# Performance work log

Hardware: AMD Instinct MI355X
Metric: run time of the kernel (lower is better)

## Reference

```python
import jax, jax.numpy as jnp
import numpy as np

B, L, C, R = 8192, 49, 512, 128  # L = 7*7 hardcoded in module
H = W = 7


def _conv2d(x, w, b, pad):
    # x: (B, Cin, H, W), w: (Cout, Cin, k, k)
    y = jax.lax.conv_general_dilated(
        x, w, window_strides=(1, 1), padding=[(pad, pad), (pad, pad)],
        dimension_numbers=("NCHW", "OIHW", "NCHW"))
    return y + b[None, :, None, None]


def _star_relu(x, scale, bias):
    r = jnp.maximum(x, 0.0)
    return scale * (r * r) + bias


def setup_inputs() -> dict:
    key = jax.random.key(0)
    ks = jax.random.split(key, 12)
    s = 0.05
    return {
        "x": jax.random.normal(ks[0], (B, L, C), jnp.float32),
        "g_reduce_w": jax.random.normal(ks[1], (R, C), jnp.float32) * s,
        "l_reduce_w": jax.random.normal(ks[2], (R, C), jnp.float32) * s,
        "conv3_w": jax.random.normal(ks[3], (R // 2, R // 2, 3, 3), jnp.float32) * s,
        "conv3_b": jax.random.normal(ks[4], (R // 2,), jnp.float32) * s,
        "conv5_w": jax.random.normal(ks[5], (R - R // 2, R - R // 2, 5, 5), jnp.float32) * s,
        "conv5_b": jax.random.normal(ks[6], (R - R // 2,), jnp.float32) * s,
        "channel_w": jax.random.normal(ks[7], (C, R), jnp.float32) * s,
        "channel_b": jax.random.normal(ks[8], (C,), jnp.float32) * s,
        "spatial_w": jax.random.normal(ks[9], (1, 3 * R), jnp.float32) * s,
        "spatial_b": jax.random.normal(ks[10], (1,), jnp.float32) * s,
        "star_scale": jnp.ones((1,), jnp.float32),
        "star_bias": jnp.zeros((1,), jnp.float32),
    }


def reference(x, g_reduce_w, l_reduce_w, conv3_w, conv3_b, conv5_w, conv5_b,
              channel_w, channel_b, spatial_w, spatial_b, star_scale, star_bias):
    # x: (B, L, C) with L = 49 (7x7)
    # Global dual pooling over spatial (== over L)
    x_max = jnp.max(x, axis=1)   # (B, C)
    x_avg = jnp.mean(x, axis=1)  # (B, C)
    # g_reduce 1x1 conv (no bias) + StarReLU
    g1 = _star_relu(x_max @ g_reduce_w.T, star_scale, star_bias)  # (B, R)
    g2 = _star_relu(x_avg @ g_reduce_w.T, star_scale, star_bias)  # (B, R)
    # Local branch: 1x1 reduce -> HybConv2d (split 3x3 / 5x5) -> StarReLU
    x_img = x.transpose(0, 2, 1).reshape(B, C, H, W)
    x_l = jnp.einsum("bchw,rc->brhw", x_img, l_reduce_w)  # (B, R, 7, 7)
    xl1, xl2 = x_l[:, :R // 2], x_l[:, R // 2:]
    y1 = _conv2d(xl1, conv3_w, conv3_b, pad=1)
    y2 = _conv2d(xl2, conv5_w, conv5_b, pad=2)
    x_l = _star_relu(jnp.concatenate([y1, y2], axis=1), star_scale, star_bias)
    x_l = x_l.reshape(B, R, L).transpose(0, 2, 1)  # (B, L, R)
    # Channel gate: Linear(R->C) applied to each pooled branch, summed
    c_aggr = jax.nn.sigmoid((g1 @ channel_w.T + channel_b)
                            + (g2 @ channel_w.T + channel_b))  # (B, C)
    # Spatial gate: concat [x_l, g1 broadcast, g2 broadcast] -> Linear(3R->1)
    g1b = jnp.broadcast_to(g1[:, None, :], (B, L, R))
    g2b = jnp.broadcast_to(g2[:, None, :], (B, L, R))
    s_cat = jnp.concatenate([x_l, g1b, g2b], axis=-1)  # (B, L, 3R)
    s_aggr = jax.nn.sigmoid(jnp.einsum("blk,ok->blo", s_cat, spatial_w) + spatial_b)  # (B, L, 1)
    aggr = c_aggr[:, None, :] * s_aggr  # (B, L, C)
    return x * aggr
```

## Files before the change

### kernel.cpp

```cpp
#include <hip/hip_runtime.h>
#include <math.h>

#define B_ 8192
#define L_ 49
#define C_ 512
#define R_ 128

typedef short   bf16x8 __attribute__((ext_vector_type(8)));
typedef unsigned short u16x8 __attribute__((ext_vector_type(8)));
typedef float   f32x4  __attribute__((ext_vector_type(4)));

#define WS_LWF   0
#define WS_WB3F  65536
#define WS_WB5F  102400
#define WS_GWF   204800
#define WS_CWF   270336

#define SM_XB    0
#define SM_XLB   25088
#define SM_MAXB  25088
#define SM_SUMF  29184
#define SM_GA    37888
#define SM_G     38912
#define SM_CA    39936
#define SM_SPW   41984
#define SM_SP    44032
#define SM_GDOT  44288
#define SM_TOT   44304

__device__ __forceinline__ float bf2f(unsigned short u) {
    union { float f; unsigned int i; } v; v.i = ((unsigned int)u) << 16; return v.f;
}
__device__ __forceinline__ unsigned short f2bf(float f) {
    union { float f; unsigned int i; } v; v.f = f;
    unsigned int r = v.i + 0x7fffu + ((v.i >> 16) & 1u);
    return (unsigned short)(r >> 16);
}
__device__ __forceinline__ float star_relu(float x, float sc, float bi) {
    float r = fmaxf(x, 0.f);
    return sc * r * r + bi;
}
__device__ __forceinline__ float sigmoidf_(float x) {
    return 1.f / (1.f + __expf(-x));
}

__global__ void cvt_weights(const float* __restrict__ lw, const float* __restrict__ w3,
                            const float* __restrict__ w5, const float* __restrict__ gw,
                            const float* __restrict__ cw, unsigned short* __restrict__ ws)
{
    int t = blockIdx.x * blockDim.x + threadIdx.x;
    int stride = gridDim.x * blockDim.x;
    for (int i = t; i < 65536; i += stride) {
        int j = i & 7, lane = (i >> 3) & 63, ks = (i >> 9) & 15, nt = i >> 13;
        int n = nt * 16 + (lane & 15);
        int k = ks * 32 + (lane >> 4) * 8 + j;
        ws[WS_LWF + i] = f2bf(lw[n * 512 + k]);
        ws[WS_GWF + i] = f2bf(gw[n * 512 + k]);
    }
    for (int i = t; i < 65536; i += stride) {
        int j = i & 7, c = (i >> 3) & 511, r8 = i >> 12;
        ws[WS_CWF + i] = f2bf(cw[c * 128 + r8 * 8 + j]);
    }
    for (int i = t; i < 36864; i += stride) {
        int j = i & 7, lane = (i >> 3) & 63, ks = (i >> 9) & 1, f = (i >> 10) & 3, tap = i >> 12;
        int oc = f * 16 + (lane & 15);
        int ic = ks * 32 + (lane >> 4) * 8 + j;
        ws[WS_WB3F + i] = f2bf(w3[(oc * 64 + ic) * 9 + tap]);
    }
    for (int i = t; i < 102400; i += stride) {
        int j = i & 7, lane = (i >> 3) & 63, ks = (i >> 9) & 1, f = (i >> 10) & 3, tap = i >> 12;
        int oc = f * 16 + (lane & 15);
        int ic = ks * 32 + (lane >> 4) * 8 + j;
        ws[WS_WB5F + i] = f2bf(w5[(oc * 64 + ic) * 25 + tap]);
    }
}

template <int NTAP, int KD, int PAD, int COLBASE>
__device__ __forceinline__ void conv_mfma(const unsigned short* __restrict__ s_xlb,
                                          const unsigned short* __restrict__ wtbf,
                                          int m16, int kg, int ln, int f, f32x4 C[4])
{
    int lp_[4], i_[4], j_[4];
    #pragma unroll
    for (int mf = 0; mf < 4; ++mf) {
        lp_[mf] = mf * 16 + m16;
        i_[mf] = lp_[mf] / 7;
        j_[mf] = lp_[mf] % 7;
    }
    bf16x8 cur0 = *(const bf16x8*)(wtbf + ((0 * 4 + f) * 2 + 0) * 512 + ln * 8);
    bf16x8 cur1 = *(const bf16x8*)(wtbf + ((0 * 4 + f) * 2 + 1) * 512 + ln * 8);
    #pragma unroll
    for (int tap = 0; tap < NTAP; ++tap) {
        bf16x8 nxt0 = cur0, nxt1 = cur1;
        if (tap + 1 < NTAP) {
            nxt0 = *(const bf16x8*)(wtbf + (((tap + 1) * 4 + f) * 2 + 0) * 512 + ln * 8);
            nxt1 = *(const bf16x8*)(wtbf + (((tap + 1) * 4 + f) * 2 + 1) * 512 + ln * 8);
        }
        const int dy = tap / KD - PAD, dx = tap % KD - PAD;
        int lc[4];
        #pragma unroll
        for (int mf = 0; mf < 4; ++mf) {
            int ii = i_[mf] + dy, jj = j_[mf] + dx;
            bool v = (lp_[mf] < 49) & (ii >= 0) & (ii < 7) & (jj >= 0) & (jj < 7);
            lc[mf] = v ? (ii * 7 + jj) : 49;
        }
        #pragma unroll
        for (int mf = 0; mf < 4; ++mf) {
            int chunk0 = ((COLBASE >> 3) + kg) ^ (lc[mf] & 7);
            bf16x8 a = *(const bf16x8*)&s_xlb[lc[mf] * 128 + chunk0 * 8];
            C[mf] = __builtin_amdgcn_mfma_f32_16x16x32_bf16(a, cur0, C[mf], 0, 0, 0);
        }
        #pragma unroll
        for (int mf = 0; mf < 4; ++mf) {
            int chunk1 = ((COLBASE >> 3) + 4 + kg) ^ (lc[mf] & 7);
            bf16x8 a = *(const bf16x8*)&s_xlb[lc[mf] * 128 + chunk1 * 8];
            C[mf] = __builtin_amdgcn_mfma_f32_16x16x32_bf16(a, cur1, C[mf], 0, 0, 0);
        }
        cur0 = nxt0; cur1 = nxt1;
    }
}

__global__ __launch_bounds__(512, 4)
void mafn_fused(const float* __restrict__ x,
                const float* __restrict__ b3, const float* __restrict__ b5,
                const float* __restrict__ cb, const float* __restrict__ sw,
                const float* __restrict__ sb, const float* __restrict__ ssc,
                const float* __restrict__ sbi,
                const unsigned short* __restrict__ ws,
                float* __restrict__ out)
{
    __shared__ __align__(16) unsigned char smem[SM_TOT];
    unsigned short* s_xb   = (unsigned short*)(smem + SM_XB);
    unsigned short* s_xlb  = (unsigned short*)(smem + SM_XLB);
    unsigned short* s_maxb = (unsigned short*)(smem + SM_MAXB);
    float*          s_sumf = (float*)(smem + SM_SUMF);
    unsigned short* s_ga   = (unsigned short*)(smem + SM_GA);
    float*          s_g    = (float*)(smem + SM_G);
    float*          s_ca   = (float*)(smem + SM_CA);
    float*          s_spw  = (float*)(smem + SM_SPW);
    float*          s_sp   = (float*)(smem + SM_SP);
    float*          s_gdot = (float*)(smem + SM_GDOT);

    const int b = blockIdx.x, t = threadIdx.x;
    const int wv = t >> 6, ln = t & 63;
    const int m16 = ln & 15, kg = ln >> 4;
    const float scale = ssc[0], sbias = sbi[0];

    const unsigned short* lwf  = ws + WS_LWF;
    const unsigned short* wb3f = ws + WS_WB3F;
    const unsigned short* wb5f = ws + WS_WB5F;
    const unsigned short* gwf  = ws + WS_GWF;
    const unsigned short* cwf  = ws + WS_CWF;

    f32x4 accA[4];
    f32x4 accG;
    {
        const f32x4 z = {0.f, 0.f, 0.f, 0.f};
        #pragma unroll
        for (int mf = 0; mf < 4; ++mf) accA[mf] = z;
        accG = z;
    }

    const int l0 = wv * 6;
    const int nl = (wv < 7) ? 6 : 7;

    #pragma unroll 1
    for (int h = 0; h < 2; ++h) {
        {
            const float4* x4 = (const float4*)(x + (size_t)b * (L_ * C_)) + h * 64;
            float4 mx = {-3.4e38f, -3.4e38f, -3.4e38f, -3.4e38f};
            float4 sm = {0.f, 0.f, 0.f, 0.f};
            for (int li = 0; li < nl; ++li) {
                int l = l0 + li;
                float4 v = x4[l * 128 + ln];
                mx.x = fmaxf(mx.x, v.x); mx.y = fmaxf(mx.y, v.y);
                mx.z = fmaxf(mx.z, v.z); mx.w = fmaxf(mx.w, v.w);
                sm.x += v.x; sm.y += v.y; sm.z += v.z; sm.w += v.w;
                ushort4 p;
                p.x = f2bf(v.x); p.y = f2bf(v.y); p.z = f2bf(v.z); p.w = f2bf(v.w);
                int chunk = (ln >> 1) ^ (l & 7);
                *(ushort4*)&s_xb[l * 256 + chunk * 8 + (ln & 1) * 4] = p;
            }
            ushort4 pm;
            pm.x = f2bf(mx.x); pm.y = f2bf(mx.y); pm.z = f2bf(mx.z); pm.w = f2bf(mx.w);
            *(ushort4*)&s_maxb[wv * 256 + ln * 4] = pm;
            *(float4*)&s_sumf[wv * 256 + ln * 4] = sm;
        }
        __syncthreads();

        {
            if (t < 256) {
                int c = t;
                float m = bf2f(s_maxb[c]);
                #pragma unroll
                for (int i = 1; i < 8; ++i) m = fmaxf(m, bf2f(s_maxb[i * 256 + c]));
                s_ga[c] = f2bf(m);
            } else {
                int c = t - 256;
                float s = 0.f;
                #pragma unroll
                for (int i = 0; i < 8; ++i) s += s_sumf[i * 256 + c];
                s_ga[256 + c] = f2bf(s * (1.f / 49.f));
            }
        }
        __syncthreads();

        {
            int rowA[4];
            #pragma unroll
            for (int mf = 0; mf < 4; ++mf) rowA[mf] = min(mf * 16 + m16, 48);

            bf16x8 bb0 = *(const bf16x8*)(lwf + (wv * 16 + h * 8 + 0) * 512 + ln * 8);
            bf16x8 bb1 = *(const bf16x8*)(lwf + (wv * 16 + h * 8 + 1) * 512 + ln * 8);
            #pragma unroll
            for (int ks = 0; ks < 8; ++ks) {
                bf16x8 bn = bb1;
                if (ks + 2 < 8)
                    bn = *(const bf16x8*)(lwf + (wv * 16 + h * 8 + ks + 2) * 512 + ln * 8);
                #pragma unroll
                for (int mf = 0; mf < 4; ++mf) {
                    int chunk = (ks * 4 + kg) ^ (rowA[mf] & 7);
                    bf16x8 a = *(const bf16x8*)&s_xb[rowA[mf] * 256 + chunk * 8];
                    accA[mf] = __builtin_amdgcn_mfma_f32_16x16x32_bf16(a, bb0, accA[mf], 0, 0, 0);
                }
                bb0 = bb1; bb1 = bn;
            }

            bf16x8 gb0 = *(const bf16x8*)(gwf + (wv * 16 + h * 8 + 0) * 512 + ln * 8);
            bf16x8 gb1 = *(const bf16x8*)(gwf + (wv * 16 + h * 8 + 1) * 512 + ln * 8);
            const bf16x8 zz = {0,0,0,0,0,0,0,0};
            #pragma unroll
            for (int ks = 0; ks < 8; ++ks) {
                bf16x8 gn = gb1;
                if (ks + 2 < 8)
                    gn = *(const bf16x8*)(gwf + (wv * 16 + h * 8 + ks + 2) * 512 + ln * 8);
                bf16x8 a = (m16 < 2) ? *(const bf16x8*)&s_ga[m16 * 256 + ks * 32 + kg * 8] : zz;
                accG = __builtin_amdgcn_mfma_f32_16x16x32_bf16(a, gb0, accG, 0, 0, 0);
                gb0 = gb1; gb1 = gn;
            }
        }
        __syncthreads();
    }

    {
        if (t < 64) ((unsigned int*)(s_xlb + 49 * 128))[t] = 0;
        const int n = wv * 16 + m16;
        #pragma unroll
        for (int mf = 0; mf < 4; ++mf) {
            #pragma unroll
            for (int rg = 0; rg < 4; ++rg) {
                int lp = mf * 16 + kg * 4 + rg;
                if (lp < 49) {
                    int idx = lp * 128 + ((((n >> 3) ^ (lp & 7)) << 3) + (n & 7));
                    s_xlb[idx] = f2bf(accA[mf][rg]);
                }
            }
        }
        if (kg == 0) {
            s_g[n]       = star_relu(accG[0], scale, sbias);
            s_g[128 + n] = star_relu(accG[1], scale, sbias);
        }
    }
    __syncthreads();

    const int f_ = wv & 3;
    const int oc_ = f_ * 16 + m16;
    {
        f32x4 C[4];
        const f32x4 z = {0.f, 0.f, 0.f, 0.f};
        #pragma unroll
        for (int mf = 0; mf < 4; ++mf) C[mf] = z;

        if (wv < 4) {
            conv_mfma<25, 5, 2, 64>(s_xlb, wb5f, m16, kg, ln, f_, C);
        } else {
            conv_mfma< 9, 3, 1,  0>(s_xlb, wb3f, m16, kg, ln, f_, C);
            const int idx = t - 256;
            #pragma unroll
            for (int half = 0; half < 2; ++half) {
                int c = idx + half * 256;
                float a0 = 0.f, a1 = 0.f;
                #pragma unroll 4
                for (int r8 = 0; r8 < 16; ++r8) {
                    u16x8 w = *(const u16x8*)(cwf + r8 * 4096 + c * 8);
                    float p = 0.f;
                    #pragma unroll
                    for (int k = 0; k < 8; ++k)
                        p += bf2f(w[k]) * (s_g[r8 * 8 + k] + s_g[128 + r8 * 8 + k]);
                    if (r8 & 1) a1 += p; else a0 += p;
                }
                s_ca[c] = sigmoidf_(a0 + a1 + 2.f * cb[c]);
            }
            if (wv == 7) {
                float p = s_g[ln] * sw[128 + ln] + s_g[128 + ln] * sw[256 + ln]
                        + s_g[ln + 64] * sw[128 + ln + 64] + s_g[128 + ln + 64] * sw[256 + ln + 64];
                #pragma unroll
                for (int off = 32; off > 0; off >>= 1) p += __shfl_xor(p, off);
                if (ln == 0) s_gdot[0] = p;
            }
        }

        const bool is5 = (wv < 4);
        const int ch = is5 ? 64 + oc_ : oc_;
        const float bias = is5 ? b5[oc_] : b3[oc_];
        const float sww = sw[ch];
        #pragma unroll
        for (int mf = 0; mf < 4; ++mf) {
            #pragma unroll
            for (int rg = 0; rg < 4; ++rg) {
                int lp = mf * 16 + kg * 4 + rg;
                float v = (lp < 49) ? star_relu(C[mf][rg] + bias, scale, sbias) * sww : 0.f;
                v += __shfl_xor(v, 1);
                v += __shfl_xor(v, 2);
                v += __shfl_xor(v, 4);
                v += __shfl_xor(v, 8);
                if (m16 == 0 && lp < 49) s_spw[wv * 64 + lp] = v;
            }
        }
    }
    __syncthreads();

    if (t < 49) {
        float s = s_gdot[0] + sb[0];
        #pragma unroll
        for (int w = 0; w < 8; ++w) s += s_spw[w * 64 + t];
        s_sp[t] = sigmoidf_(s);
    }
    __syncthreads();

    {
        const float4* x4 = (const float4*)(x + (size_t)b * (L_ * C_));
        float4* o4 = (float4*)(out + (size_t)b * (L_ * C_));
        const float4* ca4 = (const float4*)s_ca;
        for (int i = t; i < 49 * 128; i += 512) {
            int l = i >> 7, c4 = i & 127;
            float4 xv = x4[i];
            float g = s_sp[l];
            float4 cv = ca4[c4];
            float4 ov;
            ov.x = xv.x * cv.x * g;
            ov.y = xv.y * cv.y * g;
            ov.z = xv.z * cv.z * g;
            ov.w = xv.w * cv.w * g;
            o4[i] = ov;
        }
    }
}

extern "C" void kernel_launch(void* const* d_in, const int* in_sizes, int n_in,
                              void* d_out, int out_size, void* d_ws, size_t ws_size,
                              hipStream_t stream) {
    (void)in_sizes; (void)n_in; (void)ws_size; (void)out_size;
    const float* x    = (const float*)d_in[0];
    const float* g_w  = (const float*)d_in[1];
    const float* l_w  = (const float*)d_in[2];
    const float* w3   = (const float*)d_in[3];
    const float* b3   = (const float*)d_in[4];
    const float* w5   = (const float*)d_in[5];
    const float* b5   = (const float*)d_in[6];
    const float* cw   = (const float*)d_in[7];
    const float* cb   = (const float*)d_in[8];
    const float* sw   = (const float*)d_in[9];
    const float* sb   = (const float*)d_in[10];
    const float* ssc  = (const float*)d_in[11];
    const float* sbi  = (const float*)d_in[12];
    float* outp = (float*)d_out;
    unsigned short* ws = (unsigned short*)d_ws;

    cvt_weights<<<dim3(512), dim3(256), 0, stream>>>(l_w, w3, w5, g_w, cw, ws);
    mafn_fused<<<dim3(B_), dim3(512), 0, stream>>>(
        x, b3, b5, cb, sw, sb, ssc, sbi, ws, outp);
}
```

Baseline: 648.2 us.

## Stage full 512-channel tile in LDS in one pass instead of two halves

```diff
diff --git a/kernel.cpp b/kernel.cpp
--- a/kernel.cpp
+++ b/kernel.cpp
@@ -16,17 +16,17 @@
 #define WS_GWF   204800
 #define WS_CWF   270336
 
+#define SM_G     0
+#define SM_CA    1024
+#define SM_SPW   3072
+#define SM_SP    5120
+#define SM_GDOT  5376
 #define SM_XB    0
-#define SM_XLB   25088
-#define SM_MAXB  25088
-#define SM_SUMF  29184
-#define SM_GA    37888
-#define SM_G     38912
-#define SM_CA    39936
-#define SM_SPW   41984
-#define SM_SP    44032
-#define SM_GDOT  44288
-#define SM_TOT   44304
+#define SM_XLB   50176
+#define SM_MAXB  50176
+#define SM_SUMF  54272
+#define SM_GA    62976
+#define SM_TOT   65024
 
 __device__ __forceinline__ float bf2f(unsigned short u) {
     union { float f; unsigned int i; } v; v.i = ((unsigned int)u) << 16; return v.f;
@@ -161,86 +161,79 @@
         accG = z;
     }
 
-    const int l0 = wv * 6;
-    const int nl = (wv < 7) ? 6 : 7;
-
-    #pragma unroll 1
-    for (int h = 0; h < 2; ++h) {
-        {
-            const float4* x4 = (const float4*)(x + (size_t)b * (L_ * C_)) + h * 64;
-            float4 mx = {-3.4e38f, -3.4e38f, -3.4e38f, -3.4e38f};
-            float4 sm = {0.f, 0.f, 0.f, 0.f};
-            for (int li = 0; li < nl; ++li) {
-                int l = l0 + li;
-                float4 v = x4[l * 128 + ln];
-                mx.x = fmaxf(mx.x, v.x); mx.y = fmaxf(mx.y, v.y);
-                mx.z = fmaxf(mx.z, v.z); mx.w = fmaxf(mx.w, v.w);
-                sm.x += v.x; sm.y += v.y; sm.z += v.z; sm.w += v.w;
-                ushort4 p;
-                p.x = f2bf(v.x); p.y = f2bf(v.y); p.z = f2bf(v.z); p.w = f2bf(v.w);
-                int chunk = (ln >> 1) ^ (l & 7);
-                *(ushort4*)&s_xb[l * 256 + chunk * 8 + (ln & 1) * 4] = p;
-            }
-            ushort4 pm;
-            pm.x = f2bf(mx.x); pm.y = f2bf(mx.y); pm.z = f2bf(mx.z); pm.w = f2bf(mx.w);
-            *(ushort4*)&s_maxb[wv * 256 + ln * 4] = pm;
-            *(float4*)&s_sumf[wv * 256 + ln * 4] = sm;
-        }
-        __syncthreads();
-
-        {
-            if (t < 256) {
-                int c = t;
-                float m = bf2f(s_maxb[c]);
-                #pragma unroll
-                for (int i = 1; i < 8; ++i) m = fmaxf(m, bf2f(s_maxb[i * 256 + c]));
-                s_ga[c] = f2bf(m);
-            } else {
-                int c = t - 256;
-                float s = 0.f;
-                #pragma unroll
-                for (int i = 0; i < 8; ++i) s += s_sumf[i * 256 + c];
-                s_ga[256 + c] = f2bf(s * (1.f / 49.f));
-            }
-        }
-        __syncthreads();
-
-        {
-            int rowA[4];
+    {
+        const float4* x4 = (const float4*)(x + (size_t)b * (L_ * C_));
+        const int c4 = t & 127, rg = t >> 7;
+        const int l0 = rg * 12;
+        const int nl = (rg < 3) ? 12 : 13;
+        float4 mx = {-3.4e38f, -3.4e38f, -3.4e38f, -3.4e38f};
+        float4 sm = {0.f, 0.f, 0.f, 0.f};
+        for (int li = 0; li < nl; ++li) {
+            int l = l0 + li;
+            float4 v = x4[l * 128 + c4];
+            mx.x = fmaxf(mx.x, v.x); mx.y = fmaxf(mx.y, v.y);
+            mx.z = fmaxf(mx.z, v.z); mx.w = fmaxf(mx.w, v.w);
+            sm.x += v.x; sm.y += v.y; sm.z += v.z; sm.w += v.w;
+            ushort4 p;
+            p.x = f2bf(v.x); p.y = f2bf(v.y); p.z = f2bf(v.z); p.w = f2bf(v.w);
+            int chunk = (c4 >> 1) ^ (l & 7);
+            *(ushort4*)&s_xb[l * 512 + chunk * 8 + (c4 & 1) * 4] = p;
+        }
+        ushort4 pm;
+        pm.x = f2bf(mx.x); pm.y = f2bf(mx.y); pm.z = f2bf(mx.z); pm.w = f2bf(mx.w);
+        *(ushort4*)&s_maxb[rg * 512 + c4 * 4] = pm;
+        *(float4*)&s_sumf[rg * 512 + c4 * 4] = sm;
+    }
+    __syncthreads();
+
+    {
+        int c = t;
+        float m = bf2f(s_maxb[c]);
+        #pragma unroll
+        for (int i = 1; i < 4; ++i) m = fmaxf(m, bf2f(s_maxb[i * 512 + c]));
+        float s = 0.f;
+        #pragma unroll
+        for (int i = 0; i < 4; ++i) s += s_sumf[i * 512 + c];
+        s_ga[c] = f2bf(m);
+        s_ga[512 + c] = f2bf(s * (1.f / 49.f));
+    }
+    __syncthreads();
+
+    {
+        int rowA[4];
+        #pragma unroll
+        for (int mf = 0; mf < 4; ++mf) rowA[mf] = min(mf * 16 + m16, 48);
+
+        bf16x8 bb0 = *(const bf16x8*)(lwf + (wv * 16 + 0) * 512 + ln * 8);
+        bf16x8 bb1 = *(const bf16x8*)(lwf + (wv * 16 + 1) * 512 + ln * 8);
+        #pragma unroll
+        for (int ks = 0; ks < 16; ++ks) {
+            bf16x8 bn = bb1;
+            if (ks + 2 < 16)
+                bn = *(const bf16x8*)(lwf + (wv * 16 + ks + 2) * 512 + ln * 8);
             #pragma unroll
-            for (int mf = 0; mf < 4; ++mf) rowA[mf] = min(mf * 16 + m16, 48);
-
-            bf16x8 bb0 = *(const bf16x8*)(lwf + (wv * 16 + h * 8 + 0) * 512 + ln * 8);
-            bf16x8 bb1 = *(const bf16x8*)(lwf + (wv * 16 + h * 8 + 1) * 512 + ln * 8);
-            #pragma unroll
-            for (int ks = 0; ks < 8; ++ks) {
-                bf16x8 bn = bb1;
-                if (ks + 2 < 8)
-                    bn = *(const bf16x8*)(lwf + (wv * 16 + h * 8 + ks + 2) * 512 + ln * 8);
-                #pragma unroll
-                for (int mf = 0; mf < 4; ++mf) {
-                    int chunk = (ks * 4 + kg) ^ (rowA[mf] & 7);
-                    bf16x8 a = *(const bf16x8*)&s_xb[rowA[mf] * 256 + chunk * 8];
-                    accA[mf] = __builtin_amdgcn_mfma_f32_16x16x32_bf16(a, bb0, accA[mf], 0, 0, 0);
-                }
-                bb0 = bb1; bb1 = bn;
-            }
-
-            bf16x8 gb0 = *(const bf16x8*)(gwf + (wv * 16 + h * 8 + 0) * 512 + ln * 8);
-            bf16x8 gb1 = *(const bf16x8*)(gwf + (wv * 16 + h * 8 + 1) * 512 + ln * 8);
-            const bf16x8 zz = {0,0,0,0,0,0,0,0};
-            #pragma unroll
-            for (int ks = 0; ks < 8; ++ks) {
-                bf16x8 gn = gb1;
-                if (ks + 2 < 8)
-                    gn = *(const bf16x8*)(gwf + (wv * 16 + h * 8 + ks + 2) * 512 + ln * 8);
-                bf16x8 a = (m16 < 2) ? *(const bf16x8*)&s_ga[m16 * 256 + ks * 32 + kg * 8] : zz;
-                accG = __builtin_amdgcn_mfma_f32_16x16x32_bf16(a, gb0, accG, 0, 0, 0);
-                gb0 = gb1; gb1 = gn;
-            }
-        }
-        __syncthreads();
-    }
+            for (int mf = 0; mf < 4; ++mf) {
+                int chunk = (ks * 4 + kg) ^ (rowA[mf] & 7);
+                bf16x8 a = *(const bf16x8*)&s_xb[rowA[mf] * 512 + chunk * 8];
+                accA[mf] = __builtin_amdgcn_mfma_f32_16x16x32_bf16(a, bb0, accA[mf], 0, 0, 0);
+            }
+            bb0 = bb1; bb1 = bn;
+        }
+
+        bf16x8 gb0 = *(const bf16x8*)(gwf + (wv * 16 + 0) * 512 + ln * 8);
+        bf16x8 gb1 = *(const bf16x8*)(gwf + (wv * 16 + 1) * 512 + ln * 8);
+        const bf16x8 zz = {0,0,0,0,0,0,0,0};
+        #pragma unroll
+        for (int ks = 0; ks < 16; ++ks) {
+            bf16x8 gn = gb1;
+            if (ks + 2 < 16)
+                gn = *(const bf16x8*)(gwf + (wv * 16 + ks + 2) * 512 + ln * 8);
+            bf16x8 a = (m16 < 2) ? *(const bf16x8*)&s_ga[m16 * 512 + ks * 32 + kg * 8] : zz;
+            accG = __builtin_amdgcn_mfma_f32_16x16x32_bf16(a, gb0, accG, 0, 0, 0);
+            gb0 = gb1; gb1 = gn;
+        }
+    }
+    __syncthreads();
 
     {
         if (t < 64) ((unsigned int*)(s_xlb + 49 * 128))[t] = 0;
@@ -331,12 +324,12 @@
     {
         const float4* x4 = (const float4*)(x + (size_t)b * (L_ * C_));
         float4* o4 = (float4*)(out + (size_t)b * (L_ * C_));
-        const float4* ca4 = (const float4*)s_ca;
+        const int c4 = t & 127;
+        const float4 cv = *(const float4*)&s_ca[c4 * 4];
         for (int i = t; i < 49 * 128; i += 512) {
-            int l = i >> 7, c4 = i & 127;
+            int l = i >> 7;
             float4 xv = x4[i];
             float g = s_sp[l];
-            float4 cv = ca4[c4];
             float4 ov;
             ov.x = xv.x * cv.x * g;
             ov.y = xv.y * cv.y * g;
```

Result: faster. 602.2 us (median of 3 runs) (-7.1%).
